# Optimization experiments

Measured on AMD Instinct MI355X. Metric: run time of the kernel, lower is better.

The kernel has to match this reference:

```python
import jax, jax.numpy as jnp
import numpy as np

N, E, IN, H = 10000, 320000, 128, 64

def setup_inputs() -> dict:
    key = jax.random.key(0)
    ks = jax.random.split(key, 6)
    x = jax.random.normal(ks[0], (N, IN), dtype=jnp.float32)
    edge_index = jax.random.randint(ks[1], (2, E), 0, N)
    edge_weight = jax.random.uniform(ks[2], (E,), dtype=jnp.float32)
    W_rel = jax.random.normal(ks[3], (IN, H), dtype=jnp.float32) / np.float32(np.sqrt(IN))
    W_root = jax.random.normal(ks[4], (IN, H), dtype=jnp.float32) / np.float32(np.sqrt(IN))
    b = jnp.zeros((H,), dtype=jnp.float32)
    return {"x": x, "edge_index": edge_index, "edge_weight": edge_weight,
            "W_rel": W_rel, "W_root": W_root, "b": b}

def reference(x, edge_index, edge_weight, W_rel, W_root, b):
    # GraphConv (PyG): out_i = W_rel @ sum_{j->i} e_ji * x_j + W_root @ x_i + b
    src, dst = edge_index[0], edge_index[1]
    msgs = x[src] * edge_weight[:, None]                    # [E, IN] gather
    agg = jax.ops.segment_sum(msgs, dst, num_segments=N)    # [N, IN] scatter-add
    z = agg @ W_rel + x @ W_root + b                        # [N, H]
    # (activation=None, dropout inactive in eval, no BN)
    adj = jax.nn.sigmoid(z @ z.T)                           # [N, N] inner-product decoder
    return adj, z
```

## Files before the change

### kernel.cpp

```cpp
#include <hip/hip_runtime.h>
#include <hip/hip_bf16.h>
#include <stdint.h>

#define N_NODES 10000
#define N_EDGES 320000
#define DIM_IN  128
#define DIM_H   64
#define SSTR    72
#define CSTR    132

typedef __attribute__((ext_vector_type(8))) short  short8;
typedef __attribute__((ext_vector_type(8))) unsigned short ushort8;
typedef __attribute__((ext_vector_type(4))) float  f32x4;

__device__ __forceinline__ unsigned short f2bf(float f) {
    union { float f; unsigned int i; } v; v.f = f;
    unsigned int u = v.i;
    return (unsigned short)((u + 0x7fffu + ((u >> 16) & 1u)) >> 16);
}

__global__ void hist_kernel(const int* __restrict__ ei, int* __restrict__ deg) {
    int e = blockIdx.x * blockDim.x + threadIdx.x;
    if (e < N_EDGES) atomicAdd(&deg[ei[N_EDGES + e]], 1);
}

__global__ void __launch_bounds__(1024) scan_kernel(const int* __restrict__ deg,
                                                    int* __restrict__ offs,
                                                    int* __restrict__ cursor) {
    __shared__ int part[1024];
    int t = threadIdx.x;
    int base = t * 10;
    int local[10];
    int s = 0;
    for (int i = 0; i < 10; ++i) {
        int idx = base + i;
        int d = (idx < N_NODES) ? deg[idx] : 0;
        local[i] = d; s += d;
    }
    part[t] = s;
    __syncthreads();
    for (int o = 1; o < 1024; o <<= 1) {
        int add = (t >= o) ? part[t - o] : 0;
        __syncthreads();
        part[t] += add;
        __syncthreads();
    }
    int run = part[t] - s;
    for (int i = 0; i < 10; ++i) {
        int idx = base + i;
        if (idx < N_NODES) { offs[idx] = run; cursor[idx] = run; run += local[i]; }
    }
    if (t == 1023) offs[N_NODES] = part[1023];
}

__global__ void bucket_kernel(const int* __restrict__ ei,
                              const float* __restrict__ ew,
                              int* __restrict__ cursor,
                              int2* __restrict__ swsrt) {
    int e = blockIdx.x * blockDim.x + threadIdx.x;
    if (e < N_EDGES) {
        int d = ei[N_EDGES + e];
        int slot = atomicAdd(&cursor[d], 1);
        int2 pay;
        pay.x = ei[e];
        pay.y = __float_as_int(ew[e]);
        swsrt[slot] = pay;
    }
}

__global__ void __launch_bounds__(64) feat_kernel(
    const float* __restrict__ x,
    const float* __restrict__ wrel,
    const float* __restrict__ wroot,
    const float* __restrict__ bias,
    float* __restrict__ xr,
    float* __restrict__ xw)
{
    int i = blockIdx.x;
    int lane = threadIdx.x;
    __shared__ float xL[DIM_IN];
    float2 xi = ((const float2*)(x + (size_t)i * DIM_IN))[lane];
    xL[2 * lane]     = xi.x;
    xL[2 * lane + 1] = xi.y;
    __syncthreads();

    float ar = 0.f, aw = bias[lane];
    for (int k = 0; k < DIM_IN; ++k) {
        float xv = xL[k];
        ar += xv * wrel[k * DIM_H + lane];
        aw += xv * wroot[k * DIM_H + lane];
    }
    xr[(size_t)i * DIM_H + lane] = ar;
    xw[(size_t)i * DIM_H + lane] = aw;
}

__global__ void __launch_bounds__(64) agg_kernel(
    const float* __restrict__ xr,
    const float* __restrict__ xw,
    const int2* __restrict__ swsrt,
    const int* __restrict__ offs,
    float* __restrict__ out,
    unsigned short* __restrict__ zb)
{
    int i = blockIdx.x;
    int lane = threadIdx.x;
    int q   = lane >> 4;
    int l16 = lane & 15;

    int beg = offs[i], end = offs[i + 1];
    f32x4 a = (f32x4)0.f;
    #pragma unroll 4
    for (int p = beg + q; p < end; p += 4) {
        int2 sw = swsrt[p];
        float w = __int_as_float(sw.y);
        f32x4 v = *(const f32x4*)(xr + (size_t)sw.x * DIM_H + l16 * 4);
        a += v * w;
    }
    f32x4 b;
    b.x = __shfl_xor(a.x, 16); b.y = __shfl_xor(a.y, 16);
    b.z = __shfl_xor(a.z, 16); b.w = __shfl_xor(a.w, 16);
    a += b;
    b.x = __shfl_xor(a.x, 32); b.y = __shfl_xor(a.y, 32);
    b.z = __shfl_xor(a.z, 32); b.w = __shfl_xor(a.w, 32);
    a += b;

    if (q == 0) {
        f32x4 w4 = *(const f32x4*)(xw + (size_t)i * DIM_H + l16 * 4);
        f32x4 z4 = a + w4;
        *(f32x4*)(out + (size_t)N_NODES * N_NODES + (size_t)i * DIM_H + l16 * 4) = z4;
        ushort4 h;
        h.x = f2bf(z4.x); h.y = f2bf(z4.y); h.z = f2bf(z4.z); h.w = f2bf(z4.w);
        *(ushort4*)(zb + (size_t)i * DIM_H + l16 * 4) = h;
    }
}

__global__ void __launch_bounds__(256) gemm_sig_kernel(
    const unsigned short* __restrict__ zb, float* __restrict__ out)
{
    __shared__ __align__(16) unsigned short sAB[2 * 128 * SSTR];
    unsigned short* sA = sAB;
    unsigned short* sB = sAB + 128 * SSTR;

    int t    = threadIdx.x;
    int lane = t & 63;
    int wave = t >> 6;
    int wm = wave >> 1, wn = wave & 1;
    int j0 = blockIdx.x * 128;
    int i0 = blockIdx.y * 128;
    int l15  = lane & 15;
    int quad = lane >> 4;

    #pragma unroll
    for (int pass = 0; pass < 4; ++pass) {
        int c   = pass * 256 + t;
        int row = c >> 3;
        int c8  = (c & 7) << 3;
        int ga = i0 + row; if (ga >= N_NODES) ga = N_NODES - 1;
        int gb = j0 + row; if (gb >= N_NODES) gb = N_NODES - 1;
        ushort8 va = *(const ushort8*)(zb + (size_t)ga * DIM_H + c8);
        ushort8 vb = *(const ushort8*)(zb + (size_t)gb * DIM_H + c8);
        *(ushort8*)(&sA[row * SSTR + c8]) = va;
        *(ushort8*)(&sB[row * SSTR + c8]) = vb;
    }
    __syncthreads();

    f32x4 acc[4][4];
    #pragma unroll
    for (int a = 0; a < 4; ++a)
        #pragma unroll
        for (int b = 0; b < 4; ++b) acc[a][b] = (f32x4)0.f;

    #pragma unroll
    for (int s = 0; s < 2; ++s) {
        int kb = quad * 8 + s * 32;
        short8 af[4], bfr[4];
        #pragma unroll
        for (int mi = 0; mi < 4; ++mi)
            af[mi] = *(const short8*)(&sA[(wm * 64 + mi * 16 + l15) * SSTR + kb]);
        #pragma unroll
        for (int ni = 0; ni < 4; ++ni)
            bfr[ni] = *(const short8*)(&sB[(wn * 64 + ni * 16 + l15) * SSTR + kb]);
        #pragma unroll
        for (int mi = 0; mi < 4; ++mi)
            #pragma unroll
            for (int ni = 0; ni < 4; ++ni)
                acc[mi][ni] = __builtin_amdgcn_mfma_f32_16x16x32_bf16(
                    af[mi], bfr[ni], acc[mi][ni], 0, 0, 0);
    }

    float* sC = (float*)sAB;
    #pragma unroll
    for (int half = 0; half < 2; ++half) {
        __syncthreads();
        if (wm == half) {
            #pragma unroll
            for (int mi = 0; mi < 4; ++mi)
                #pragma unroll
                for (int ni = 0; ni < 4; ++ni)
                    #pragma unroll
                    for (int r = 0; r < 4; ++r)
                        sC[(mi * 16 + quad * 4 + r) * CSTR + wn * 64 + ni * 16 + l15]
                            = acc[mi][ni][r];
        }
        __syncthreads();
        int i0h = i0 + half * 64;
        #pragma unroll
        for (int it = 0; it < 8; ++it) {
            int idx = it * 256 + t;
            int row = idx >> 5;
            int c4  = (idx & 31) << 2;
            f32x4 v = *(const f32x4*)&sC[row * CSTR + c4];
            f32x4 sg;
            sg.x = 1.0f / (1.0f + __expf(-v.x));
            sg.y = 1.0f / (1.0f + __expf(-v.y));
            sg.z = 1.0f / (1.0f + __expf(-v.z));
            sg.w = 1.0f / (1.0f + __expf(-v.w));
            int grow = i0h + row;
            int gcol = j0 + c4;
            if (grow < N_NODES && gcol + 3 < N_NODES) {
                __builtin_nontemporal_store(
                    sg, (f32x4*)(out + (size_t)grow * N_NODES + gcol));
            }
        }
    }
}

extern "C" void kernel_launch(void* const* d_in, const int* in_sizes, int n_in,
                              void* d_out, int out_size, void* d_ws, size_t ws_size,
                              hipStream_t stream) {
    const float* x     = (const float*)d_in[0];
    const int*   ei    = (const int*)d_in[1];
    const float* ew    = (const float*)d_in[2];
    const float* wrel  = (const float*)d_in[3];
    const float* wroot = (const float*)d_in[4];
    const float* bias  = (const float*)d_in[5];
    float* out = (float*)d_out;

    char* base = (char*)d_ws;
    unsigned short* zb = (unsigned short*)(base);
    float* xr    = (float*)(base + 1280000);
    float* xw    = (float*)(base + 3840000);
    int2* swsrt  = (int2*)(base + 6400000);
    int* deg     = (int*)(base + 8960000);
    int* offs    = (int*)(base + 9000000);
    int* cursor  = (int*)(base + 9040004);

    hipMemsetAsync(deg, 0, N_NODES * sizeof(int), stream);
    hist_kernel<<<(N_EDGES + 255) / 256, 256, 0, stream>>>(ei, deg);
    scan_kernel<<<1, 1024, 0, stream>>>(deg, offs, cursor);
    bucket_kernel<<<(N_EDGES + 255) / 256, 256, 0, stream>>>(ei, ew, cursor, swsrt);
    feat_kernel<<<N_NODES, 64, 0, stream>>>(x, wrel, wroot, bias, xr, xw);
    agg_kernel<<<N_NODES, 64, 0, stream>>>(xr, xw, swsrt, offs, out, zb);
    dim3 grid((N_NODES + 127) / 128, (N_NODES + 127) / 128);
    gemm_sig_kernel<<<grid, 256, 0, stream>>>(zb, out);
}
```

Before: 499.6 us.

## Fuse graph preprocessing and aggregation into one cooperative persistent kernel

Replaces the memset and the five separate kernels (histogram, scan, bucket, feature transform, aggregation) with a single cooperative kernel that uses grid.sync between phases. The goal is to remove per-launch overhead and gaps between the small kernels. In exchange, phases run with a fixed 1024-block grid separated by grid-wide barriers, and the scan still runs on only one block while the rest of the grid waits. The deg zeroing happens before the feature phase and is separated from the histogram by a grid sync, so it stays correct.

```diff
diff --git a/kernel.cpp b/kernel.cpp
--- a/kernel.cpp
+++ b/kernel.cpp
@@ -1,6 +1,9 @@
 #include <hip/hip_runtime.h>
 #include <hip/hip_bf16.h>
+#include <hip/hip_cooperative_groups.h>
 #include <stdint.h>
+
+namespace cg = cooperative_groups;
 
 #define N_NODES 10000
 #define N_EDGES 320000
@@ -8,6 +11,8 @@
 #define DIM_H   64
 #define SSTR    72
 #define CSTR    132
+#define PBLOCKS 1024
+#define PTHREADS 256
 
 typedef __attribute__((ext_vector_type(8))) short  short8;
 typedef __attribute__((ext_vector_type(8))) unsigned short ushort8;
@@ -19,46 +24,86 @@
     return (unsigned short)((u + 0x7fffu + ((u >> 16) & 1u)) >> 16);
 }
 
-__global__ void hist_kernel(const int* __restrict__ ei, int* __restrict__ deg) {
-    int e = blockIdx.x * blockDim.x + threadIdx.x;
-    if (e < N_EDGES) atomicAdd(&deg[ei[N_EDGES + e]], 1);
-}
-
-__global__ void __launch_bounds__(1024) scan_kernel(const int* __restrict__ deg,
-                                                    int* __restrict__ offs,
-                                                    int* __restrict__ cursor) {
-    __shared__ int part[1024];
-    int t = threadIdx.x;
-    int base = t * 10;
-    int local[10];
-    int s = 0;
-    for (int i = 0; i < 10; ++i) {
-        int idx = base + i;
-        int d = (idx < N_NODES) ? deg[idx] : 0;
-        local[i] = d; s += d;
-    }
-    part[t] = s;
-    __syncthreads();
-    for (int o = 1; o < 1024; o <<= 1) {
-        int add = (t >= o) ? part[t - o] : 0;
-        __syncthreads();
-        part[t] += add;
-        __syncthreads();
-    }
-    int run = part[t] - s;
-    for (int i = 0; i < 10; ++i) {
-        int idx = base + i;
-        if (idx < N_NODES) { offs[idx] = run; cursor[idx] = run; run += local[i]; }
-    }
-    if (t == 1023) offs[N_NODES] = part[1023];
-}
-
-__global__ void bucket_kernel(const int* __restrict__ ei,
-                              const float* __restrict__ ew,
-                              int* __restrict__ cursor,
-                              int2* __restrict__ swsrt) {
-    int e = blockIdx.x * blockDim.x + threadIdx.x;
-    if (e < N_EDGES) {
+__global__ void __launch_bounds__(PTHREADS) prologue_kernel(
+    const float* __restrict__ x,
+    const int*   __restrict__ ei,
+    const float* __restrict__ ew,
+    const float* __restrict__ wrel,
+    const float* __restrict__ wroot,
+    const float* __restrict__ bias,
+    float*       __restrict__ out,
+    unsigned short* __restrict__ zb,
+    float*       __restrict__ xr,
+    float*       __restrict__ xw,
+    int2*        __restrict__ swsrt,
+    int*         __restrict__ deg,
+    int*         __restrict__ offs,
+    int*         __restrict__ cursor)
+{
+    cg::grid_group grid = cg::this_grid();
+    __shared__ float xLs[4][DIM_IN];
+    __shared__ int   part[PTHREADS];
+
+    int t    = threadIdx.x;
+    int wave = t >> 6;
+    int lane = t & 63;
+    int gid  = blockIdx.x * PTHREADS + t;
+
+    if (gid < N_NODES) deg[gid] = 0;
+    for (int base = blockIdx.x * 4; base < N_NODES; base += PBLOCKS * 4) {
+        int node = base + wave;
+        int nc = node < N_NODES ? node : N_NODES - 1;
+        float2 xi = ((const float2*)(x + (size_t)nc * DIM_IN))[lane];
+        xLs[wave][2 * lane]     = xi.x;
+        xLs[wave][2 * lane + 1] = xi.y;
+        __syncthreads();
+        float ar = 0.f, aw = bias[lane];
+        for (int k = 0; k < DIM_IN; ++k) {
+            float xv = xLs[wave][k];
+            ar += xv * wrel[k * DIM_H + lane];
+            aw += xv * wroot[k * DIM_H + lane];
+        }
+        if (node < N_NODES) {
+            xr[(size_t)node * DIM_H + lane] = ar;
+            xw[(size_t)node * DIM_H + lane] = aw;
+        }
+        __syncthreads();
+    }
+    grid.sync();
+
+    for (int e = gid; e < N_EDGES; e += PBLOCKS * PTHREADS)
+        atomicAdd(&deg[ei[N_EDGES + e]], 1);
+    grid.sync();
+
+    if (blockIdx.x == 0) {
+        const int PER = 40;
+        int base = t * PER;
+        int s = 0;
+        for (int k = 0; k < PER; ++k) {
+            int idx = base + k;
+            if (idx < N_NODES) s += deg[idx];
+        }
+        part[t] = s;
+        __syncthreads();
+        for (int o = 1; o < PTHREADS; o <<= 1) {
+            int add = (t >= o) ? part[t - o] : 0;
+            __syncthreads();
+            part[t] += add;
+            __syncthreads();
+        }
+        int run = part[t] - s;
+        for (int k = 0; k < PER; ++k) {
+            int idx = base + k;
+            if (idx < N_NODES) {
+                int d = deg[idx];
+                offs[idx] = run; cursor[idx] = run; run += d;
+            }
+        }
+        if (t == PTHREADS - 1) offs[N_NODES] = part[PTHREADS - 1];
+    }
+    grid.sync();
+
+    for (int e = gid; e < N_EDGES; e += PBLOCKS * PTHREADS) {
         int d = ei[N_EDGES + e];
         int slot = atomicAdd(&cursor[d], 1);
         int2 pay;
@@ -66,71 +111,35 @@
         pay.y = __float_as_int(ew[e]);
         swsrt[slot] = pay;
     }
-}
-
-__global__ void __launch_bounds__(64) feat_kernel(
-    const float* __restrict__ x,
-    const float* __restrict__ wrel,
-    const float* __restrict__ wroot,
-    const float* __restrict__ bias,
-    float* __restrict__ xr,
-    float* __restrict__ xw)
-{
-    int i = blockIdx.x;
-    int lane = threadIdx.x;
-    __shared__ float xL[DIM_IN];
-    float2 xi = ((const float2*)(x + (size_t)i * DIM_IN))[lane];
-    xL[2 * lane]     = xi.x;
-    xL[2 * lane + 1] = xi.y;
-    __syncthreads();
-
-    float ar = 0.f, aw = bias[lane];
-    for (int k = 0; k < DIM_IN; ++k) {
-        float xv = xL[k];
-        ar += xv * wrel[k * DIM_H + lane];
-        aw += xv * wroot[k * DIM_H + lane];
-    }
-    xr[(size_t)i * DIM_H + lane] = ar;
-    xw[(size_t)i * DIM_H + lane] = aw;
-}
-
-__global__ void __launch_bounds__(64) agg_kernel(
-    const float* __restrict__ xr,
-    const float* __restrict__ xw,
-    const int2* __restrict__ swsrt,
-    const int* __restrict__ offs,
-    float* __restrict__ out,
-    unsigned short* __restrict__ zb)
-{
-    int i = blockIdx.x;
-    int lane = threadIdx.x;
+    grid.sync();
+
     int q   = lane >> 4;
     int l16 = lane & 15;
-
-    int beg = offs[i], end = offs[i + 1];
-    f32x4 a = (f32x4)0.f;
-    #pragma unroll 4
-    for (int p = beg + q; p < end; p += 4) {
-        int2 sw = swsrt[p];
-        float w = __int_as_float(sw.y);
-        f32x4 v = *(const f32x4*)(xr + (size_t)sw.x * DIM_H + l16 * 4);
-        a += v * w;
-    }
-    f32x4 b;
-    b.x = __shfl_xor(a.x, 16); b.y = __shfl_xor(a.y, 16);
-    b.z = __shfl_xor(a.z, 16); b.w = __shfl_xor(a.w, 16);
-    a += b;
-    b.x = __shfl_xor(a.x, 32); b.y = __shfl_xor(a.y, 32);
-    b.z = __shfl_xor(a.z, 32); b.w = __shfl_xor(a.w, 32);
-    a += b;
-
-    if (q == 0) {
-        f32x4 w4 = *(const f32x4*)(xw + (size_t)i * DIM_H + l16 * 4);
-        f32x4 z4 = a + w4;
-        *(f32x4*)(out + (size_t)N_NODES * N_NODES + (size_t)i * DIM_H + l16 * 4) = z4;
-        ushort4 h;
-        h.x = f2bf(z4.x); h.y = f2bf(z4.y); h.z = f2bf(z4.z); h.w = f2bf(z4.w);
-        *(ushort4*)(zb + (size_t)i * DIM_H + l16 * 4) = h;
+    for (int i = blockIdx.x * 4 + wave; i < N_NODES; i += PBLOCKS * 4) {
+        int beg = offs[i], end = offs[i + 1];
+        f32x4 a = (f32x4)0.f;
+        #pragma unroll 4
+        for (int p = beg + q; p < end; p += 4) {
+            int2 sw = swsrt[p];
+            float w = __int_as_float(sw.y);
+            f32x4 v = *(const f32x4*)(xr + (size_t)sw.x * DIM_H + l16 * 4);
+            a += v * w;
+        }
+        f32x4 b;
+        b.x = __shfl_xor(a.x, 16); b.y = __shfl_xor(a.y, 16);
+        b.z = __shfl_xor(a.z, 16); b.w = __shfl_xor(a.w, 16);
+        a += b;
+        b.x = __shfl_xor(a.x, 32); b.y = __shfl_xor(a.y, 32);
+        b.z = __shfl_xor(a.z, 32); b.w = __shfl_xor(a.w, 32);
+        a += b;
+        if (q == 0) {
+            f32x4 w4 = *(const f32x4*)(xw + (size_t)i * DIM_H + l16 * 4);
+            f32x4 z4 = a + w4;
+            *(f32x4*)(out + (size_t)N_NODES * N_NODES + (size_t)i * DIM_H + l16 * 4) = z4;
+            ushort4 h;
+            h.x = f2bf(z4.x); h.y = f2bf(z4.y); h.z = f2bf(z4.z); h.w = f2bf(z4.w);
+            *(ushort4*)(zb + (size_t)i * DIM_H + l16 * 4) = h;
+        }
     }
 }
 
@@ -245,12 +254,15 @@
     int* offs    = (int*)(base + 9000000);
     int* cursor  = (int*)(base + 9040004);
 
-    hipMemsetAsync(deg, 0, N_NODES * sizeof(int), stream);
-    hist_kernel<<<(N_EDGES + 255) / 256, 256, 0, stream>>>(ei, deg);
-    scan_kernel<<<1, 1024, 0, stream>>>(deg, offs, cursor);
-    bucket_kernel<<<(N_EDGES + 255) / 256, 256, 0, stream>>>(ei, ew, cursor, swsrt);
-    feat_kernel<<<N_NODES, 64, 0, stream>>>(x, wrel, wroot, bias, xr, xw);
-    agg_kernel<<<N_NODES, 64, 0, stream>>>(xr, xw, swsrt, offs, out, zb);
+    void* pargs[] = {
+        (void*)&x, (void*)&ei, (void*)&ew, (void*)&wrel, (void*)&wroot,
+        (void*)&bias, (void*)&out, (void*)&zb, (void*)&xr, (void*)&xw,
+        (void*)&swsrt, (void*)&deg, (void*)&offs, (void*)&cursor
+    };
+    (void)hipLaunchCooperativeKernel((void*)prologue_kernel,
+                                     dim3(PBLOCKS), dim3(PTHREADS),
+                                     pargs, 0, stream);
+
     dim3 grid((N_NODES + 127) / 128, (N_NODES + 127) / 128);
     gemm_sig_kernel<<<grid, 256, 0, stream>>>(zb, out);
 }
```

New measurement: 980.6 us. 1.96x slower.

## Exploit symmetry of z·zᵀ: compute upper-triangular tiles and write transposed mirror

Applied to the files above, without the earlier changes.

The decoder GEMM grid now covers only the upper-triangular 128x128 tiles, mapped from a 1D block index through a closed-form triangular inverse. Off-diagonal blocks also write the transposed tile, read from shared memory with the row stride padded to 133 to limit bank conflicts. This roughly halves the MFMA work and operand loads, but output bytes are unchanged and the kernel is likely bound by its 400MB of writes. The deg memset is also folded into feat_kernel, which now runs first and removes one memset launch.

```diff
diff --git a/kernel.cpp b/kernel.cpp
--- a/kernel.cpp
+++ b/kernel.cpp
@@ -6,8 +6,9 @@
 #define N_EDGES 320000
 #define DIM_IN  128
 #define DIM_H   64
+#define NT      79
 #define SSTR    72
-#define CSTR    132
+#define CSTR    133
 
 typedef __attribute__((ext_vector_type(8))) short  short8;
 typedef __attribute__((ext_vector_type(8))) unsigned short ushort8;
@@ -17,6 +18,35 @@
     union { float f; unsigned int i; } v; v.f = f;
     unsigned int u = v.i;
     return (unsigned short)((u + 0x7fffu + ((u >> 16) & 1u)) >> 16);
+}
+
+__global__ void __launch_bounds__(64) feat_kernel(
+    const float* __restrict__ x,
+    const float* __restrict__ wrel,
+    const float* __restrict__ wroot,
+    const float* __restrict__ bias,
+    float* __restrict__ xr,
+    float* __restrict__ xw,
+    int*   __restrict__ deg)
+{
+    int i = blockIdx.x;
+    int lane = threadIdx.x;
+    if (lane == 0) deg[i] = 0;
+
+    __shared__ float xL[DIM_IN];
+    float2 xi = ((const float2*)(x + (size_t)i * DIM_IN))[lane];
+    xL[2 * lane]     = xi.x;
+    xL[2 * lane + 1] = xi.y;
+    __syncthreads();
+
+    float ar = 0.f, aw = bias[lane];
+    for (int k = 0; k < DIM_IN; ++k) {
+        float xv = xL[k];
+        ar += xv * wrel[k * DIM_H + lane];
+        aw += xv * wroot[k * DIM_H + lane];
+    }
+    xr[(size_t)i * DIM_H + lane] = ar;
+    xw[(size_t)i * DIM_H + lane] = aw;
 }
 
 __global__ void hist_kernel(const int* __restrict__ ei, int* __restrict__ deg) {
@@ -68,32 +98,6 @@
     }
 }
 
-__global__ void __launch_bounds__(64) feat_kernel(
-    const float* __restrict__ x,
-    const float* __restrict__ wrel,
-    const float* __restrict__ wroot,
-    const float* __restrict__ bias,
-    float* __restrict__ xr,
-    float* __restrict__ xw)
-{
-    int i = blockIdx.x;
-    int lane = threadIdx.x;
-    __shared__ float xL[DIM_IN];
-    float2 xi = ((const float2*)(x + (size_t)i * DIM_IN))[lane];
-    xL[2 * lane]     = xi.x;
-    xL[2 * lane + 1] = xi.y;
-    __syncthreads();
-
-    float ar = 0.f, aw = bias[lane];
-    for (int k = 0; k < DIM_IN; ++k) {
-        float xv = xL[k];
-        ar += xv * wrel[k * DIM_H + lane];
-        aw += xv * wroot[k * DIM_H + lane];
-    }
-    xr[(size_t)i * DIM_H + lane] = ar;
-    xw[(size_t)i * DIM_H + lane] = aw;
-}
-
 __global__ void __launch_bounds__(64) agg_kernel(
     const float* __restrict__ xr,
     const float* __restrict__ xw,
@@ -145,10 +149,18 @@
     int lane = t & 63;
     int wave = t >> 6;
     int wm = wave >> 1, wn = wave & 1;
-    int j0 = blockIdx.x * 128;
-    int i0 = blockIdx.y * 128;
     int l15  = lane & 15;
     int quad = lane >> 4;
+
+    int bid = blockIdx.x;
+    int bi = (int)floorf((float)NT + 0.5f -
+                         sqrtf(((float)NT + 0.5f) * ((float)NT + 0.5f) - 2.0f * bid));
+    if (bi < 0) bi = 0;
+    while (bi * NT - bi * (bi - 1) / 2 > bid) --bi;
+    while ((bi + 1) * NT - (bi + 1) * bi / 2 <= bid) ++bi;
+    int bj = bi + (bid - (bi * NT - bi * (bi - 1) / 2));
+    int i0 = bi * 128;
+    int j0 = bj * 128;
 
     #pragma unroll
     for (int pass = 0; pass < 4; ++pass) {
@@ -204,6 +216,7 @@
         }
         __syncthreads();
         int i0h = i0 + half * 64;
+
         #pragma unroll
         for (int it = 0; it < 8; ++it) {
             int idx = it * 256 + t;
@@ -222,6 +235,31 @@
                     sg, (f32x4*)(out + (size_t)grow * N_NODES + gcol));
             }
         }
+
+        if (bi != bj) {
+            #pragma unroll
+            for (int it = 0; it < 8; ++it) {
+                int idx  = it * 256 + t;
+                int mrow = idx >> 4;
+                int mc4  = (idx & 15) << 2;
+                f32x4 v;
+                v.x = sC[(mc4 + 0) * CSTR + mrow];
+                v.y = sC[(mc4 + 1) * CSTR + mrow];
+                v.z = sC[(mc4 + 2) * CSTR + mrow];
+                v.w = sC[(mc4 + 3) * CSTR + mrow];
+                f32x4 sg;
+                sg.x = 1.0f / (1.0f + __expf(-v.x));
+                sg.y = 1.0f / (1.0f + __expf(-v.y));
+                sg.z = 1.0f / (1.0f + __expf(-v.z));
+                sg.w = 1.0f / (1.0f + __expf(-v.w));
+                int grow = j0 + mrow;
+                int gcol = i0h + mc4;
+                if (grow < N_NODES && gcol + 3 < N_NODES) {
+                    __builtin_nontemporal_store(
+                        sg, (f32x4*)(out + (size_t)grow * N_NODES + gcol));
+                }
+            }
+        }
     }
 }
 
@@ -245,12 +283,10 @@
     int* offs    = (int*)(base + 9000000);
     int* cursor  = (int*)(base + 9040004);
 
-    hipMemsetAsync(deg, 0, N_NODES * sizeof(int), stream);
+    feat_kernel<<<N_NODES, 64, 0, stream>>>(x, wrel, wroot, bias, xr, xw, deg);
     hist_kernel<<<(N_EDGES + 255) / 256, 256, 0, stream>>>(ei, deg);
     scan_kernel<<<1, 1024, 0, stream>>>(deg, offs, cursor);
     bucket_kernel<<<(N_EDGES + 255) / 256, 256, 0, stream>>>(ei, ew, cursor, swsrt);
-    feat_kernel<<<N_NODES, 64, 0, stream>>>(x, wrel, wroot, bias, xr, xw);
     agg_kernel<<<N_NODES, 64, 0, stream>>>(xr, xw, swsrt, offs, out, zb);
-    dim3 grid((N_NODES + 127) / 128, (N_NODES + 127) / 128);
-    gemm_sig_kernel<<<grid, 256, 0, stream>>>(zb, out);
-}
+    gemm_sig_kernel<<<NT * (NT + 1) / 2, 256, 0, stream>>>(zb, out);
+}
```

Result: slower. 515.6 us (+3.2%).
